# Kernel optimization log

Measured on AMD Instinct MI355X. Metric: run time of the kernel, lower is better.

## Reference

```python
import jax, jax.numpy as jnp
import numpy as np

B, S, D, H = 2048, 64, 512, 8
HD = D // H
SCALE = float(1.0 / np.sqrt(HD))


def _static_masks():
    # 6 static chess relations over the 8x8 board: file, rank, diagonal,
    # anti-diagonal, knight (+self), king (8-neighborhood +self)
    sq = np.arange(64)
    r = sq // 8
    f = sq % 8
    ri, rj = r[:, None], r[None, :]
    fi, fj = f[:, None], f[None, :]
    dr = np.abs(ri - rj)
    df = np.abs(fi - fj)
    eye = np.eye(64, dtype=bool)
    file_m = fi == fj
    rank_m = ri == rj
    diag_m = (ri - fi) == (rj - fj)
    adiag_m = (ri + fi) == (rj + fj)
    knight_m = (((dr == 2) & (df == 1)) | ((dr == 1) & (df == 2))) | eye
    king_m = (dr <= 1) & (df <= 1)  # includes self
    return np.stack([file_m, rank_m, diag_m, adiag_m, knight_m, king_m])


STATIC = jnp.asarray(_static_masks())  # (6, 64, 64) bool
EYE = jnp.eye(S, dtype=bool)


def setup_inputs() -> dict:
    key = jax.random.key(0)
    ks = jax.random.split(key, 7)
    x = jax.random.normal(ks[0], (B, S, D), jnp.float32)
    # dynamic per-board masks (head 6 = unobstructed sliding rays, head 7 = attacks)
    ray_mask = jax.random.bernoulli(ks[1], 0.15, (B, S, S))
    attack_mask = jax.random.bernoulli(ks[2], 0.10, (B, S, S))
    s = 1.0 / np.sqrt(D)

    def lin(k):
        k1, k2 = jax.random.split(k)
        W = jax.random.uniform(k1, (D, D), jnp.float32, -s, s)
        b = jax.random.uniform(k2, (D,), jnp.float32, -s, s)
        return W, b

    Wq, bq = lin(ks[3])
    Wk, bk = lin(ks[4])
    Wv, bv = lin(ks[5])
    Wo, bo = lin(ks[6])
    return dict(x=x, ray_mask=ray_mask, attack_mask=attack_mask,
                Wq=Wq, bq=bq, Wk=Wk, bk=bk, Wv=Wv, bv=bv, Wo=Wo, bo=bo)


def reference(x, ray_mask, attack_mask, Wq, bq, Wk, bk, Wv, bv, Wo, bo):
    Bn = x.shape[0]

    def split_heads(t):  # (B, S, D) -> (B, H, S, HD)
        return t.reshape(Bn, S, H, HD).transpose(0, 2, 1, 3)

    q = split_heads(x @ Wq.T + bq)
    k = split_heads(x @ Wk.T + bk)
    v = split_heads(x @ Wv.T + bv)

    scores = jnp.einsum('bhsd,bhtd->bhst', q, k) * SCALE  # (B, H, 64, 64)

    # per-head topology: heads 0-5 static relations, head 6 ray, head 7 attack;
    # dynamic masks get self-connections OR-ed in
    mask = jnp.concatenate([
        jnp.broadcast_to(STATIC[None], (Bn, 6, S, S)),
        (ray_mask | EYE)[:, None],
        (attack_mask | EYE)[:, None],
    ], axis=1)  # (B, 8, 64, 64) bool

    scores = jnp.where(mask, scores, jnp.float32(-1e9))
    attn = jax.nn.softmax(scores, axis=-1)
    out = jnp.einsum('bhst,bhtd->bhsd', attn, v)
    out = out.transpose(0, 2, 1, 3).reshape(Bn, S, D)
    return out @ Wo.T + bo
```

## Files before the change

kernel.cpp:

```cpp
#include <hip/hip_runtime.h>
#include <stdint.h>

typedef unsigned short u16;
typedef unsigned char u8;
typedef short bf16x8 __attribute__((ext_vector_type(8)));
typedef float f32x4 __attribute__((ext_vector_type(4)));
typedef u16 u16x4 __attribute__((ext_vector_type(4)));

#define Bn 2048
#define Sn 64
#define Dn 512
#define Hn 8
#define MTOT (Bn*Sn)

__device__ __forceinline__ u16 f2bf(float f){
  uint32_t u = __builtin_bit_cast(uint32_t, f);
  u += 0x7FFFu + ((u>>16)&1u);
  return (u16)(u>>16);
}

__device__ __forceinline__ void gload16(const void* g, void* lds){
  __builtin_amdgcn_global_load_lds((const __attribute__((address_space(1))) void*)g,
                                   (__attribute__((address_space(3))) void*)lds, 16, 0, 0);
}

__global__ __launch_bounds__(256) void wconv_k(
    const float* __restrict__ Wq, const float* __restrict__ Wk,
    const float* __restrict__ Wv, const float* __restrict__ Wo,
    u16* __restrict__ Wqkv, u16* __restrict__ Wob)
{
  int t = blockIdx.x*256 + threadIdx.x;
  int mat = t>>16, i4 = t&65535;
  const float4* src = (mat==0)?(const float4*)Wq:(mat==1)?(const float4*)Wk:
                      (mat==2)?(const float4*)Wv:(const float4*)Wo;
  float4 v = src[i4];
  u16x4 o; o.x=f2bf(v.x); o.y=f2bf(v.y); o.z=f2bf(v.z); o.w=f2bf(v.w);
  if (mat<3) ((u16x4*)Wqkv)[t] = o;
  else       ((u16x4*)Wob)[i4] = o;
}

__global__ __launch_bounds__(256) void k1_qkv(
    const float* __restrict__ X, const u16* __restrict__ W,
    const float* __restrict__ bq, const float* __restrict__ bk, const float* __restrict__ bv,
    u16* __restrict__ Q, u16* __restrict__ Kb, u16* __restrict__ Vt)
{
  __shared__ __align__(16) u16 As[8192];
  __shared__ __align__(16) u16 Bs[8192];
  const int tid = threadIdx.x, lane = tid&63, wv = tid>>6;
  const int jbase = blockIdx.x<<7;
  const int rbase = blockIdx.y<<7;
  const int wr = (wv>>1)<<6, wc = (wv&1)<<6;
  f32x4 acc[4][4] = {};

  for (int kt=0; kt<8; ++kt){
    const float* xs = X + (size_t)rbase*Dn + kt*64;
    #pragma unroll
    for (int j=0;j<8;++j){
      int f = j*256 + tid;
      int arow = f>>4;
      int kb = (f&15)<<3;
      float4 xv = *(const float4*)(xs + (size_t)arow*Dn + (kb>>1));
      u16x4 hv; hv.x=f2bf(xv.x); hv.y=f2bf(xv.y); hv.z=f2bf(xv.z); hv.w=f2bf(xv.w);
      int off = (arow<<7) + (kb ^ ((arow&7)<<4));
      *(u16x4*)((char*)As + off) = hv;
    }
    #pragma unroll
    for (int i=0;i<4;++i){
      int chunk = (wv<<2) + i;
      int brow = (chunk<<3) + (lane>>3);
      int inner = (lane&7)<<4;
      int srcb = ((jbase + brow)<<10) + (kt<<7) + (inner ^ ((brow&7)<<4));
      gload16((const char*)W + srcb, (char*)Bs + (chunk<<10));
    }
    __syncthreads();
    bf16x8 af[4][2], bfr[4][2];
    #pragma unroll
    for (int m=0;m<4;++m){
      int row = wr + (m<<4) + (lane&15);
      #pragma unroll
      for (int kk=0;kk<2;++kk){
        int koff = ((((kk<<2)+(lane>>4)) ^ (row&7))<<4);
        af[m][kk] = *(const bf16x8*)((char*)As + (row<<7) + koff);
      }
    }
    #pragma unroll
    for (int n=0;n<4;++n){
      int row = wc + (n<<4) + (lane&15);
      #pragma unroll
      for (int kk=0;kk<2;++kk){
        int koff = ((((kk<<2)+(lane>>4)) ^ (row&7))<<4);
        bfr[n][kk] = *(const bf16x8*)((char*)Bs + (row<<7) + koff);
      }
    }
    #pragma unroll
    for (int m=0;m<4;++m)
      #pragma unroll
      for (int n=0;n<4;++n){
        acc[m][n] = __builtin_amdgcn_mfma_f32_16x16x32_bf16(af[m][0], bfr[n][0], acc[m][n], 0,0,0);
        acc[m][n] = __builtin_amdgcn_mfma_f32_16x16x32_bf16(af[m][1], bfr[n][1], acc[m][n], 0,0,0);
      }
    __syncthreads();
  }
  const int mat = jbase>>9;
  const float* bias = (mat==0)?bq:((mat==1)?bk:bv);
  u16* Out = (mat==0)?Q:((mat==1)?Kb:Vt);
  const int jb = jbase & 511;
  #pragma unroll
  for (int n=0;n<4;++n){
    int jl = jb + wc + (n<<4) + (lane&15);
    float bb = bias[jl];
    int hh = jl>>6, hd = jl&63;
    #pragma unroll
    for (int m=0;m<4;++m){
      int r0 = rbase + wr + (m<<4) + ((lane>>4)<<2);
      size_t base = ((size_t)(r0>>6)<<15) + ((size_t)hh<<12);
      if (mat==2){
        u16x4 pk;
        pk.x=f2bf(acc[m][n][0]+bb); pk.y=f2bf(acc[m][n][1]+bb);
        pk.z=f2bf(acc[m][n][2]+bb); pk.w=f2bf(acc[m][n][3]+bb);
        *(u16x4*)(Out + base + (hd<<6) + (r0&63)) = pk;
      } else {
        #pragma unroll
        for (int reg=0;reg<4;++reg){
          int r = r0+reg;
          Out[base + ((size_t)(r&63)<<6) + hd] = f2bf(acc[m][n][reg]+bb);
        }
      }
    }
  }
}

__global__ __launch_bounds__(512) void attn_k(
    u16* __restrict__ QO, const u16* __restrict__ Kb, const u16* __restrict__ Vt,
    const int* __restrict__ ray, const int* __restrict__ att)
{
  __shared__ __align__(16) u8 msk[2][4096];
  __shared__ __align__(16) u16 Plds[8][4096];
  const int b = blockIdx.x;
  const int lane = threadIdx.x&63, h = threadIdx.x>>6;
  u16* Qb = QO + ((size_t)b<<15) + (h<<12);
  const u16* Kh = Kb + ((size_t)b<<15) + (h<<12);
  const u16* Vh = Vt + ((size_t)b<<15) + (h<<12);
  if (h>=6){
    const uint4* mg = (const uint4*)((h==6?ray:att) + ((size_t)b<<12));
    #pragma unroll
    for (int j=0;j<16;++j){
      int g = (j<<6) + lane;
      uint4 w = mg[g];
      uint32_t pk = (w.x!=0u ? 1u:0u) | (w.y!=0u ? 0x100u:0u)
                  | (w.z!=0u ? 0x10000u:0u) | (w.w!=0u ? 0x1000000u:0u);
      *(uint32_t*)&msk[h-6][g<<2] = pk;
    }
  }
  const int tl = lane&15, lg = lane>>4;
  bf16x8 qf[4][2], kf[4][2];
  #pragma unroll
  for (int m=0;m<4;++m)
    #pragma unroll
    for (int kk=0;kk<2;++kk){
      int off = (((m<<4)+tl)<<6) + (kk<<5) + (lg<<3);
      qf[m][kk] = *(const bf16x8*)(Qb + off);
      kf[m][kk] = *(const bf16x8*)(Kh + off);
    }
  f32x4 sc[4][4] = {};
  #pragma unroll
  for (int m=0;m<4;++m)
    #pragma unroll
    for (int n=0;n<4;++n){
      sc[m][n] = __builtin_amdgcn_mfma_f32_16x16x32_bf16(qf[m][0], kf[n][0], sc[m][n], 0,0,0);
      sc[m][n] = __builtin_amdgcn_mfma_f32_16x16x32_bf16(qf[m][1], kf[n][1], sc[m][n], 0,0,0);
    }
  char* pw = (char*)(Plds[h]);
  #pragma unroll
  for (int m=0;m<4;++m){
    #pragma unroll
    for (int reg=0;reg<4;++reg){
      int r = (m<<4) + (lg<<2) + reg;
      int ri = r>>3, fi = r&7;
      float v4[4]; float mx = -3e38f;
      #pragma unroll
      for (int n=0;n<4;++n){
        int t = (n<<4) + tl;
        int rj = t>>3, fj = t&7;
        int dr = ri>rj?ri-rj:rj-ri, df = fi>fj?fi-fj:fj-fi;
        bool keep;
        if      (h==0) keep = (fj==fi);
        else if (h==1) keep = (rj==ri);
        else if (h==2) keep = ((ri-fi)==(rj-fj));
        else if (h==3) keep = ((ri+fi)==(rj+fj));
        else if (h==4) keep = ((dr==2&&df==1)||(dr==1&&df==2)||(r==t));
        else if (h==5) keep = (dr<=1&&df<=1);
        else           keep = (r==t) || (msk[h-6][(r<<6)+t] != 0);
        float s = keep ? sc[m][n][reg]*0.125f : -1e9f;
        v4[n] = s; mx = fmaxf(mx, s);
      }
      mx = fmaxf(mx, __shfl_xor(mx,1)); mx = fmaxf(mx, __shfl_xor(mx,2));
      mx = fmaxf(mx, __shfl_xor(mx,4)); mx = fmaxf(mx, __shfl_xor(mx,8));
      float sum = 0.f;
      #pragma unroll
      for (int n=0;n<4;++n){ float e = __expf(v4[n]-mx); v4[n]=e; sum+=e; }
      sum += __shfl_xor(sum,1); sum += __shfl_xor(sum,2);
      sum += __shfl_xor(sum,4); sum += __shfl_xor(sum,8);
      float inv = 1.0f/sum;
      #pragma unroll
      for (int n=0;n<4;++n){
        int t = (n<<4) + tl;
        int off = ((r<<7) + (t<<1)) ^ ((r&7)<<4);
        *(u16*)(pw + off) = f2bf(v4[n]*inv);
      }
    }
  }
  bf16x8 pf[4][2], vf[4][2];
  #pragma unroll
  for (int m=0;m<4;++m){
    int row = (m<<4) + tl;
    #pragma unroll
    for (int kk=0;kk<2;++kk){
      int koff = ((((kk<<2)+lg) ^ (row&7))<<4);
      pf[m][kk] = *(const bf16x8*)(pw + (row<<7) + koff);
    }
  }
  #pragma unroll
  for (int n=0;n<4;++n)
    #pragma unroll
    for (int kk=0;kk<2;++kk){
      int off = (((n<<4)+tl)<<6) + (kk<<5) + (lg<<3);
      vf[n][kk] = *(const bf16x8*)(Vh + off);
    }
  f32x4 oacc[4][4] = {};
  #pragma unroll
  for (int m=0;m<4;++m)
    #pragma unroll
    for (int n=0;n<4;++n){
      oacc[m][n] = __builtin_amdgcn_mfma_f32_16x16x32_bf16(pf[m][0], vf[n][0], oacc[m][n], 0,0,0);
      oacc[m][n] = __builtin_amdgcn_mfma_f32_16x16x32_bf16(pf[m][1], vf[n][1], oacc[m][n], 0,0,0);
    }
  #pragma unroll
  for (int m=0;m<4;++m)
    #pragma unroll
    for (int n=0;n<4;++n){
      int d = (n<<4) + tl;
      #pragma unroll
      for (int reg=0;reg<4;++reg){
        int s = (m<<4) + (lg<<2) + reg;
        Qb[(s<<6) + d] = f2bf(oacc[m][n][reg]);
      }
    }
}

__global__ __launch_bounds__(256) void k3_out(
    const u16* __restrict__ O, const u16* __restrict__ W, const float* __restrict__ bo,
    float* __restrict__ Y)
{
  __shared__ __align__(16) u16 As[8192];
  __shared__ __align__(16) u16 Bs[8192];
  const int tid = threadIdx.x, lane = tid&63, wv = tid>>6;
  const int jbase = blockIdx.x<<7;
  const int rbase = blockIdx.y<<7;
  const int wr = (wv>>1)<<6, wc = (wv&1)<<6;
  f32x4 acc[4][4] = {};
  for (int kt=0; kt<8; ++kt){
    #pragma unroll
    for (int i=0;i<4;++i){
      int chunk = (wv<<2) + i;
      int row = (chunk<<3) + (lane>>3);
      int inner = (lane&7)<<4;
      int kbyte = inner ^ ((row&7)<<4);
      int r = rbase + row;
      size_t srcA = ((size_t)(r>>6)<<15) + ((size_t)kt<<12) + ((size_t)(r&63)<<6) + (kbyte>>1);
      gload16(O + srcA, (char*)As + (chunk<<10));
      int srcB = ((jbase + row)<<10) + (kt<<7) + kbyte;
      gload16((const char*)W + srcB, (char*)Bs + (chunk<<10));
    }
    __syncthreads();
    bf16x8 af[4][2], bfr[4][2];
    #pragma unroll
    for (int m=0;m<4;++m){
      int row = wr + (m<<4) + (lane&15);
      #pragma unroll
      for (int kk=0;kk<2;++kk){
        int koff = ((((kk<<2)+(lane>>4)) ^ (row&7))<<4);
        af[m][kk] = *(const bf16x8*)((char*)As + (row<<7) + koff);
      }
    }
    #pragma unroll
    for (int n=0;n<4;++n){
      int row = wc + (n<<4) + (lane&15);
      #pragma unroll
      for (int kk=0;kk<2;++kk){
        int koff = ((((kk<<2)+(lane>>4)) ^ (row&7))<<4);
        bfr[n][kk] = *(const bf16x8*)((char*)Bs + (row<<7) + koff);
      }
    }
    #pragma unroll
    for (int m=0;m<4;++m)
      #pragma unroll
      for (int n=0;n<4;++n){
        acc[m][n] = __builtin_amdgcn_mfma_f32_16x16x32_bf16(af[m][0], bfr[n][0], acc[m][n], 0,0,0);
        acc[m][n] = __builtin_amdgcn_mfma_f32_16x16x32_bf16(af[m][1], bfr[n][1], acc[m][n], 0,0,0);
      }
    __syncthreads();
  }
  #pragma unroll
  for (int n=0;n<4;++n){
    int j = jbase + wc + (n<<4) + (lane&15);
    float bb = bo[j];
    #pragma unroll
    for (int m=0;m<4;++m){
      int r0 = rbase + wr + (m<<4) + ((lane>>4)<<2);
      #pragma unroll
      for (int reg=0;reg<4;++reg){
        Y[(size_t)(r0+reg)*Dn + j] = acc[m][n][reg] + bb;
      }
    }
  }
}

extern "C" void kernel_launch(void* const* d_in, const int* in_sizes, int n_in,
                              void* d_out, int out_size, void* d_ws, size_t ws_size,
                              hipStream_t stream) {
  const float* x   = (const float*)d_in[0];
  const int*   ray = (const int*)d_in[1];
  const int*   att = (const int*)d_in[2];
  const float* Wq  = (const float*)d_in[3];
  const float* bq  = (const float*)d_in[4];
  const float* Wk  = (const float*)d_in[5];
  const float* bk  = (const float*)d_in[6];
  const float* Wv  = (const float*)d_in[7];
  const float* bv  = (const float*)d_in[8];
  const float* Wo  = (const float*)d_in[9];
  const float* bo  = (const float*)d_in[10];

  char* ws = (char*)d_ws;
  u16* Wqkv = (u16*)ws;
  u16* Wob  = (u16*)(ws + 1572864);
  u16* Q    = (u16*)(ws + 2097152);
  u16* Kb   = (u16*)(ws + 2097152 + 134217728);
  u16* Vt   = (u16*)(ws + 2097152 + 268435456);
  float* out = (float*)d_out;

  hipLaunchKernelGGL(wconv_k, dim3(1024), dim3(256), 0, stream, Wq, Wk, Wv, Wo, Wqkv, Wob);
  hipLaunchKernelGGL(k1_qkv, dim3(12,1024), dim3(256), 0, stream, x, Wqkv, bq, bk, bv, Q, Kb, Vt);
  hipLaunchKernelGGL(attn_k, dim3(2048), dim3(512), 0, stream, Q, Kb, Vt, ray, att);
  hipLaunchKernelGGL(k3_out, dim3(4,1024), dim3(256), 0, stream, Q, Wob, bo, out);
}
```

Measured before the change: 1.238 ms.

## Pre-convert X to bf16 and remap GEMM workgroups for XCD-aware L2 locality

Adds a separate kernel that converts the fp32 input X to bf16 once, staging it in the output buffer, so the QKV GEMM can load A tiles with direct global-to-LDS loads. Previously every one of the 12 column blocks re-read and re-converted the same fp32 rows. Both GEMMs now use 1D grids with a remap that groups adjacent tiles onto the same XCD, aiming to improve L2 reuse of shared A rows. The cost is an extra pass over X (read fp32, write bf16) and reuse of d_out as scratch before k3 overwrites it.

```diff
diff --git a/kernel.cpp b/kernel.cpp
--- a/kernel.cpp
+++ b/kernel.cpp
@@ -39,38 +39,46 @@
   else       ((u16x4*)Wob)[i4] = o;
 }
 
+__global__ __launch_bounds__(256) void xconv_k(
+    const float* __restrict__ X, u16* __restrict__ Xb)
+{
+  int t = blockIdx.x*256 + threadIdx.x;
+  #pragma unroll
+  for (int i=0;i<16;++i){
+    int idx = t + i*1048576;
+    float4 v = ((const float4*)X)[idx];
+    u16x4 o; o.x=f2bf(v.x); o.y=f2bf(v.y); o.z=f2bf(v.z); o.w=f2bf(v.w);
+    ((u16x4*)Xb)[idx] = o;
+  }
+}
+
 __global__ __launch_bounds__(256) void k1_qkv(
-    const float* __restrict__ X, const u16* __restrict__ W,
+    const u16* __restrict__ Xb, const u16* __restrict__ W,
     const float* __restrict__ bq, const float* __restrict__ bk, const float* __restrict__ bv,
     u16* __restrict__ Q, u16* __restrict__ Kb, u16* __restrict__ Vt)
 {
   __shared__ __align__(16) u16 As[8192];
   __shared__ __align__(16) u16 Bs[8192];
   const int tid = threadIdx.x, lane = tid&63, wv = tid>>6;
-  const int jbase = blockIdx.x<<7;
-  const int rbase = blockIdx.y<<7;
+  const int lin = blockIdx.x;
+  const int wgid = (lin&7)*1536 + (lin>>3);
+  const int rb = wgid/12;
+  const int nt = wgid - rb*12;
+  const int jbase = nt<<7;
+  const int rbase = rb<<7;
   const int wr = (wv>>1)<<6, wc = (wv&1)<<6;
   f32x4 acc[4][4] = {};
 
   for (int kt=0; kt<8; ++kt){
-    const float* xs = X + (size_t)rbase*Dn + kt*64;
-    #pragma unroll
-    for (int j=0;j<8;++j){
-      int f = j*256 + tid;
-      int arow = f>>4;
-      int kb = (f&15)<<3;
-      float4 xv = *(const float4*)(xs + (size_t)arow*Dn + (kb>>1));
-      u16x4 hv; hv.x=f2bf(xv.x); hv.y=f2bf(xv.y); hv.z=f2bf(xv.z); hv.w=f2bf(xv.w);
-      int off = (arow<<7) + (kb ^ ((arow&7)<<4));
-      *(u16x4*)((char*)As + off) = hv;
-    }
     #pragma unroll
     for (int i=0;i<4;++i){
       int chunk = (wv<<2) + i;
-      int brow = (chunk<<3) + (lane>>3);
-      int inner = (lane&7)<<4;
-      int srcb = ((jbase + brow)<<10) + (kt<<7) + (inner ^ ((brow&7)<<4));
-      gload16((const char*)W + srcb, (char*)Bs + (chunk<<10));
+      int row = (chunk<<3) + (lane>>3);
+      int swz = ((lane&7)<<4) ^ ((row&7)<<4);
+      gload16((const char*)Xb + (((size_t)(rbase+row))<<10) + (kt<<7) + swz,
+              (char*)As + (chunk<<10));
+      gload16((const char*)W  + (((size_t)(jbase+row))<<10) + (kt<<7) + swz,
+              (char*)Bs + (chunk<<10));
     }
     __syncthreads();
     bf16x8 af[4][2], bfr[4][2];
@@ -255,8 +263,11 @@
   __shared__ __align__(16) u16 As[8192];
   __shared__ __align__(16) u16 Bs[8192];
   const int tid = threadIdx.x, lane = tid&63, wv = tid>>6;
-  const int jbase = blockIdx.x<<7;
-  const int rbase = blockIdx.y<<7;
+  const int lin = blockIdx.x;
+  const int wgid = (lin&7)*512 + (lin>>3);
+  const int nt = wgid&3, rb = wgid>>2;
+  const int jbase = nt<<7;
+  const int rbase = rb<<7;
   const int wr = (wv>>1)<<6, wc = (wv&1)<<6;
   f32x4 acc[4][4] = {};
   for (int kt=0; kt<8; ++kt){
@@ -264,12 +275,11 @@
     for (int i=0;i<4;++i){
       int chunk = (wv<<2) + i;
       int row = (chunk<<3) + (lane>>3);
-      int inner = (lane&7)<<4;
-      int kbyte = inner ^ ((row&7)<<4);
+      int kbyte = ((lane&7)<<4) ^ ((row&7)<<4);
       int r = rbase + row;
       size_t srcA = ((size_t)(r>>6)<<15) + ((size_t)kt<<12) + ((size_t)(r&63)<<6) + (kbyte>>1);
       gload16(O + srcA, (char*)As + (chunk<<10));
-      int srcB = ((jbase + row)<<10) + (kt<<7) + kbyte;
+      size_t srcB = (((size_t)(jbase + row))<<10) + (kt<<7) + kbyte;
       gload16((const char*)W + srcB, (char*)Bs + (chunk<<10));
     }
     __syncthreads();
@@ -337,10 +347,12 @@
   u16* Q    = (u16*)(ws + 2097152);
   u16* Kb   = (u16*)(ws + 2097152 + 134217728);
   u16* Vt   = (u16*)(ws + 2097152 + 268435456);
+  u16* Xb   = (u16*)d_out;
   float* out = (float*)d_out;
 
   hipLaunchKernelGGL(wconv_k, dim3(1024), dim3(256), 0, stream, Wq, Wk, Wv, Wo, Wqkv, Wob);
-  hipLaunchKernelGGL(k1_qkv, dim3(12,1024), dim3(256), 0, stream, x, Wqkv, bq, bk, bv, Q, Kb, Vt);
+  hipLaunchKernelGGL(xconv_k, dim3(4096), dim3(256), 0, stream, x, Xb);
+  hipLaunchKernelGGL(k1_qkv, dim3(12288), dim3(256), 0, stream, Xb, Wqkv, bq, bk, bv, Q, Kb, Vt);
   hipLaunchKernelGGL(attn_k, dim3(2048), dim3(512), 0, stream, Q, Kb, Vt, ray, att);
-  hipLaunchKernelGGL(k3_out, dim3(4,1024), dim3(256), 0, stream, Q, Wob, bo, out);
-}
+  hipLaunchKernelGGL(k3_out, dim3(4096), dim3(256), 0, stream, Q, Wob, bo, out);
+}
```

Result: faster. 1.182 ms (-4.5%).
